# Kernel optimization log

Measured on AMD Instinct MI355X. Metric: run time of the kernel, lower is better.

## Reference

```python
import jax, jax.numpy as jnp
import numpy as np

TEMPERATURE = 0.1
EPS = 1e-8  # torch F.cosine_similarity norm clamp


def setup_inputs() -> dict:
    key = jax.random.key(0)
    k1, k2 = jax.random.split(key)
    N, D, N_CLASSES = 4096, 512, 16
    features = jax.random.normal(k1, (N, D), dtype=jnp.float32)
    labels = jax.random.randint(k2, (N,), 0, N_CLASSES, dtype=jnp.int64)
    return {"features": features, "labels": labels}


def reference(features, labels):
    N = features.shape[0]
    # cosine similarity via normalize + matmul (same math as the broadcasted
    # F.cosine_similarity, expressed as a BLAS path)
    norms = jnp.clip(jnp.linalg.norm(features, axis=1, keepdims=True), EPS)
    f = features / norms
    sim = f @ f.T  # (N, N)

    # drop the diagonal: row i keeps columns j != i, giving (N, N-1)
    j = jnp.arange(N - 1)
    cols = j[None, :] + (j[None, :] >= jnp.arange(N)[:, None])  # (N, N-1)
    sim_nd = jnp.take_along_axis(sim, cols, axis=1)

    # positive mask: same label, diagonal excluded, same column layout
    eq = labels[:, None] == labels[None, :]
    pos_nd = jnp.take_along_axis(eq, cols, axis=1)  # (N, N-1) bool

    logits = sim_nd / TEMPERATURE
    # torch.max(mask.float(), dim=1) -> first positive index per row
    targets = jnp.argmax(pos_nd.astype(jnp.float32), axis=1)  # (N,)

    logp = jax.nn.log_softmax(logits, axis=1)
    loss = -jnp.mean(jnp.take_along_axis(logp, targets[:, None], axis=1))
    return loss
```

## Files before the change

### kernel.cpp

```cpp
#include <hip/hip_runtime.h>
#include <hip/hip_bf16.h>
#include <math.h>

#define NROW 4096
#define DIM  512
#define TINV8 0.0390625f
#define EPSN 1e-8f
#define BM 128
#define BK 64
#define NB  (NROW / BM)
#define NBLK (NB * (NB + 1) / 2)

typedef float f32x4 __attribute__((ext_vector_type(4)));

__device__ __forceinline__ void gload_lds16(const void* g, void* l) {
    __builtin_amdgcn_global_load_lds(
        (const __attribute__((address_space(1))) unsigned int*)g,
        (__attribute__((address_space(3))) unsigned int*)l,
        16, 0, 0);
}

__global__ __launch_bounds__(256) void kprep(const float* __restrict__ feat,
                                             const int* __restrict__ labels,
                                             unsigned char* __restrict__ fb8,
                                             int* __restrict__ target,
                                             float* __restrict__ rowsum) {
    if (blockIdx.x < NROW / 4) {
        const int row  = blockIdx.x * 4 + (threadIdx.x >> 6);
        const int lane = threadIdx.x & 63;
        const float* rp = feat + (size_t)row * DIM + lane * 8;
        float4 v0 = *(const float4*)rp;
        float4 v1 = *(const float4*)(rp + 4);
        float ss = v0.x*v0.x + v0.y*v0.y + v0.z*v0.z + v0.w*v0.w
                 + v1.x*v1.x + v1.y*v1.y + v1.z*v1.z + v1.w*v1.w;
        #pragma unroll
        for (int m = 1; m < 64; m <<= 1) ss += __shfl_xor(ss, m);
        const float inv = 16.0f / fmaxf(sqrtf(ss), EPSN);
        int w0 = __builtin_amdgcn_cvt_pk_fp8_f32(v0.x * inv, v0.y * inv, 0, false);
        w0     = __builtin_amdgcn_cvt_pk_fp8_f32(v0.z * inv, v0.w * inv, w0, true);
        int w1 = __builtin_amdgcn_cvt_pk_fp8_f32(v1.x * inv, v1.y * inv, 0, false);
        w1     = __builtin_amdgcn_cvt_pk_fp8_f32(v1.z * inv, v1.w * inv, w1, true);
        *(int2*)(fb8 + (size_t)row * DIM + lane * 8) = make_int2(w0, w1);
    } else {
        __shared__ int firstS[16], secondS[16];
        const int t = threadIdx.x;
        if (t < 16) { firstS[t] = NROW; secondS[t] = NROW; }
        for (int i = t; i < NROW; i += 256) rowsum[i] = 0.0f;
        __syncthreads();
        for (int i = t; i < NROW; i += 256) atomicMin(&firstS[labels[i]], i);
        __syncthreads();
        for (int i = t; i < NROW; i += 256) {
            const int c = labels[i];
            if (i != firstS[c]) atomicMin(&secondS[c], i);
        }
        __syncthreads();
        for (int i = t; i < NROW; i += 256) {
            const int c = labels[i];
            int tg = (firstS[c] == i) ? secondS[c] : firstS[c];
            if (tg >= NROW) tg = (i == 0) ? 1 : 0;
            target[i] = tg;
        }
    }
}

__global__ __launch_bounds__(256) void ksim(const unsigned char* __restrict__ fb8,
                                            const int* __restrict__ target,
                                            float* __restrict__ rowsum,
                                            float* __restrict__ tlog) {
    __shared__ __align__(16) unsigned char As[2][BM * BK];
    __shared__ __align__(16) unsigned char Bs[2][BM * BK];

    int bi = 0, rem = blockIdx.x;
    while (rem >= NB - bi) { rem -= NB - bi; bi++; }
    const int bj = bi + rem;
    const bool offdiag = (bi != bj);

    const int brow = bi * BM;
    const int bcol = bj * BM;
    const int tid  = threadIdx.x;
    const int wid  = tid >> 6;
    const int lane = tid & 63;
    const int wm = wid >> 1, wn = wid & 1;

    f32x4 acc[4][4];
    #pragma unroll
    for (int m = 0; m < 4; m++)
        #pragma unroll
        for (int n = 0; n < 4; n++)
            #pragma unroll
            for (int q = 0; q < 4; q++) acc[m][n][q] = 0.0f;

    const int skey = ((lane >> 2) & 3) ^ ((lane >> 4) & 3);
    const int sc   = (lane & 3) ^ skey;

    auto STAGE = [&](int buf, int kb) {
        #pragma unroll
        for (int q = 0; q < 2; q++) {
            const int r0 = wid * 32 + q * 16;
            const unsigned char* gA = fb8 + (size_t)(brow + r0 + (lane >> 2)) * DIM + kb + sc * 16;
            const unsigned char* gB = fb8 + (size_t)(bcol + r0 + (lane >> 2)) * DIM + kb + sc * 16;
            gload_lds16(gA, &As[buf][r0 * BK]);
            gload_lds16(gB, &Bs[buf][r0 * BK]);
        }
    };

    const int ro   = lane & 15;
    const int rkey = (ro & 3) ^ ((ro >> 2) & 3);
    const int hp   = (lane >> 4) & 1;
    const int g2   = lane >> 5;

    int cur = 0;
    STAGE(cur, 0);
    __syncthreads();

    for (int t = 0; t < DIM / BK; ++t) {
        if (t + 1 < DIM / BK) STAGE(cur ^ 1, (t + 1) * BK);
        const unsigned char* Ab = As[cur];
        const unsigned char* Bb = Bs[cur];
        #pragma unroll
        for (int kk = 0; kk < 2; kk++) {
            const int p   = (kk * 2 + g2) ^ rkey;
            const int cof = (p * 2 + hp) * 8;
            long a[4], b[4];
            #pragma unroll
            for (int m = 0; m < 4; m++)
                a[m] = *(const long*)(Ab + (wm * 64 + m * 16 + ro) * BK + cof);
            #pragma unroll
            for (int n = 0; n < 4; n++)
                b[n] = *(const long*)(Bb + (wn * 64 + n * 16 + ro) * BK + cof);
            #pragma unroll
            for (int m = 0; m < 4; m++)
                #pragma unroll
                for (int n = 0; n < 4; n++)
                    acc[m][n] = __builtin_amdgcn_mfma_f32_16x16x32_fp8_fp8(a[m], b[n], acc[m][n], 0, 0, 0);
        }
        __syncthreads();
        cur ^= 1;
    }

    const int lhi = lane >> 4, llo = lane & 15;
    float colacc[4] = {0.f, 0.f, 0.f, 0.f};
    int tgj[4];
    #pragma unroll
    for (int n = 0; n < 4; n++) tgj[n] = target[bcol + wn * 64 + n * 16 + llo];

    #pragma unroll
    for (int m = 0; m < 4; m++) {
        #pragma unroll
        for (int q = 0; q < 4; q++) {
            const int i  = brow + wm * 64 + m * 16 + lhi * 4 + q;
            const int tgi = target[i];
            float psum = 0.0f;
            #pragma unroll
            for (int n = 0; n < 4; n++) {
                const int j = bcol + wn * 64 + n * 16 + llo;
                const float logit = acc[m][n][q] * TINV8;
                const float expv  = __expf(logit);
                if (j != i) psum += expv;
                if (j == tgi) tlog[i] = logit;
                if (offdiag) {
                    colacc[n] += expv;
                    if (i == tgj[n]) tlog[j] = logit;
                }
            }
            psum += __shfl_xor(psum, 1);
            psum += __shfl_xor(psum, 2);
            psum += __shfl_xor(psum, 4);
            psum += __shfl_xor(psum, 8);
            if (llo == 0) atomicAdd(&rowsum[i], psum);
        }
    }
    if (offdiag) {
        #pragma unroll
        for (int n = 0; n < 4; n++) {
            colacc[n] += __shfl_xor(colacc[n], 16);
            colacc[n] += __shfl_xor(colacc[n], 32);
            if (lhi == 0) atomicAdd(&rowsum[bcol + wn * 64 + n * 16 + llo], colacc[n]);
        }
    }
}

__global__ __launch_bounds__(256) void kloss(const float* __restrict__ rowsum,
                                             const float* __restrict__ tlog,
                                             float* __restrict__ out) {
    __shared__ float red[256];
    float s = 0.0f;
    for (int i = threadIdx.x; i < NROW; i += 256)
        s += logf(rowsum[i]) - tlog[i];
    red[threadIdx.x] = s;
    __syncthreads();
    for (int k = 128; k > 0; k >>= 1) {
        if (threadIdx.x < k) red[threadIdx.x] += red[threadIdx.x + k];
        __syncthreads();
    }
    if (threadIdx.x == 0) out[0] = red[0] / (float)NROW;
}

extern "C" void kernel_launch(void* const* d_in, const int* in_sizes, int n_in,
                              void* d_out, int out_size, void* d_ws, size_t ws_size,
                              hipStream_t stream) {
    const float* feat  = (const float*)d_in[0];
    const int* labels  = (const int*)d_in[1];
    float* out = (float*)d_out;

    char* ws = (char*)d_ws;
    unsigned char* fb8 = (unsigned char*)ws;
    float* rowsum = (float*)(ws + (size_t)NROW * DIM);
    float* tlog   = rowsum + NROW;
    int*   target = (int*)(tlog + NROW);

    kprep<<<NROW / 4 + 1, 256, 0, stream>>>(feat, labels, fb8, target, rowsum);
    ksim <<<NBLK, 256, 0, stream>>>(fb8, target, rowsum, tlog);
    kloss<<<1, 256, 0, stream>>>(rowsum, tlog, out);
}
```

Measured before the change: 43.37 us.

## Fuse final loss reduction into similarity kernel and use 8 waves per block

```diff
diff --git a/kernel.cpp b/kernel.cpp
--- a/kernel.cpp
+++ b/kernel.cpp
@@ -24,7 +24,8 @@
                                              const int* __restrict__ labels,
                                              unsigned char* __restrict__ fb8,
                                              int* __restrict__ target,
-                                             float* __restrict__ rowsum) {
+                                             float* __restrict__ rowsum,
+                                             int* __restrict__ donecnt) {
     if (blockIdx.x < NROW / 4) {
         const int row  = blockIdx.x * 4 + (threadIdx.x >> 6);
         const int lane = threadIdx.x & 63;
@@ -45,6 +46,7 @@
         __shared__ int firstS[16], secondS[16];
         const int t = threadIdx.x;
         if (t < 16) { firstS[t] = NROW; secondS[t] = NROW; }
+        if (t == 0) *donecnt = 0;
         for (int i = t; i < NROW; i += 256) rowsum[i] = 0.0f;
         __syncthreads();
         for (int i = t; i < NROW; i += 256) atomicMin(&firstS[labels[i]], i);
@@ -63,10 +65,12 @@
     }
 }
 
-__global__ __launch_bounds__(256) void ksim(const unsigned char* __restrict__ fb8,
+__global__ __launch_bounds__(512) void ksim(const unsigned char* __restrict__ fb8,
                                             const int* __restrict__ target,
                                             float* __restrict__ rowsum,
-                                            float* __restrict__ tlog) {
+                                            float* __restrict__ tlog,
+                                            int* __restrict__ donecnt,
+                                            float* __restrict__ out) {
     __shared__ __align__(16) unsigned char As[2][BM * BK];
     __shared__ __align__(16) unsigned char Bs[2][BM * BK];
 
@@ -80,28 +84,26 @@
     const int tid  = threadIdx.x;
     const int wid  = tid >> 6;
     const int lane = tid & 63;
-    const int wm = wid >> 1, wn = wid & 1;
-
-    f32x4 acc[4][4];
+    const int wm = wid >> 2;
+    const int wn = wid & 3;
+
+    f32x4 acc[4][2];
     #pragma unroll
     for (int m = 0; m < 4; m++)
         #pragma unroll
-        for (int n = 0; n < 4; n++)
+        for (int n = 0; n < 2; n++)
             #pragma unroll
             for (int q = 0; q < 4; q++) acc[m][n][q] = 0.0f;
 
     const int skey = ((lane >> 2) & 3) ^ ((lane >> 4) & 3);
     const int sc   = (lane & 3) ^ skey;
+    const int srow = wid * 16 + (lane >> 2);
 
     auto STAGE = [&](int buf, int kb) {
-        #pragma unroll
-        for (int q = 0; q < 2; q++) {
-            const int r0 = wid * 32 + q * 16;
-            const unsigned char* gA = fb8 + (size_t)(brow + r0 + (lane >> 2)) * DIM + kb + sc * 16;
-            const unsigned char* gB = fb8 + (size_t)(bcol + r0 + (lane >> 2)) * DIM + kb + sc * 16;
-            gload_lds16(gA, &As[buf][r0 * BK]);
-            gload_lds16(gB, &Bs[buf][r0 * BK]);
-        }
+        const unsigned char* gA = fb8 + (size_t)(brow + srow) * DIM + kb + sc * 16;
+        const unsigned char* gB = fb8 + (size_t)(bcol + srow) * DIM + kb + sc * 16;
+        gload_lds16(gA, &As[buf][(wid * 16) * BK]);
+        gload_lds16(gB, &Bs[buf][(wid * 16) * BK]);
     };
 
     const int ro   = lane & 15;
@@ -121,17 +123,17 @@
         for (int kk = 0; kk < 2; kk++) {
             const int p   = (kk * 2 + g2) ^ rkey;
             const int cof = (p * 2 + hp) * 8;
-            long a[4], b[4];
+            long a[4], b[2];
             #pragma unroll
             for (int m = 0; m < 4; m++)
                 a[m] = *(const long*)(Ab + (wm * 64 + m * 16 + ro) * BK + cof);
             #pragma unroll
-            for (int n = 0; n < 4; n++)
-                b[n] = *(const long*)(Bb + (wn * 64 + n * 16 + ro) * BK + cof);
+            for (int n = 0; n < 2; n++)
+                b[n] = *(const long*)(Bb + (wn * 32 + n * 16 + ro) * BK + cof);
             #pragma unroll
             for (int m = 0; m < 4; m++)
                 #pragma unroll
-                for (int n = 0; n < 4; n++)
+                for (int n = 0; n < 2; n++)
                     acc[m][n] = __builtin_amdgcn_mfma_f32_16x16x32_fp8_fp8(a[m], b[n], acc[m][n], 0, 0, 0);
         }
         __syncthreads();
@@ -139,10 +141,10 @@
     }
 
     const int lhi = lane >> 4, llo = lane & 15;
-    float colacc[4] = {0.f, 0.f, 0.f, 0.f};
-    int tgj[4];
+    float colacc[2] = {0.f, 0.f};
+    int tgj[2];
     #pragma unroll
-    for (int n = 0; n < 4; n++) tgj[n] = target[bcol + wn * 64 + n * 16 + llo];
+    for (int n = 0; n < 2; n++) tgj[n] = target[bcol + wn * 32 + n * 16 + llo];
 
     #pragma unroll
     for (int m = 0; m < 4; m++) {
@@ -152,8 +154,8 @@
             const int tgi = target[i];
             float psum = 0.0f;
             #pragma unroll
-            for (int n = 0; n < 4; n++) {
-                const int j = bcol + wn * 64 + n * 16 + llo;
+            for (int n = 0; n < 2; n++) {
+                const int j = bcol + wn * 32 + n * 16 + llo;
                 const float logit = acc[m][n][q] * TINV8;
                 const float expv  = __expf(logit);
                 if (j != i) psum += expv;
@@ -172,28 +174,31 @@
     }
     if (offdiag) {
         #pragma unroll
-        for (int n = 0; n < 4; n++) {
+        for (int n = 0; n < 2; n++) {
             colacc[n] += __shfl_xor(colacc[n], 16);
             colacc[n] += __shfl_xor(colacc[n], 32);
-            if (lhi == 0) atomicAdd(&rowsum[bcol + wn * 64 + n * 16 + llo], colacc[n]);
-        }
-    }
-}
-
-__global__ __launch_bounds__(256) void kloss(const float* __restrict__ rowsum,
-                                             const float* __restrict__ tlog,
-                                             float* __restrict__ out) {
-    __shared__ float red[256];
+            if (lhi == 0) atomicAdd(&rowsum[bcol + wn * 32 + n * 16 + llo], colacc[n]);
+        }
+    }
+
+    __threadfence();
+    __shared__ int lastS;
+    if (tid == 0) lastS = (atomicAdd(donecnt, 1) == NBLK - 1);
+    __syncthreads();
+    if (!lastS) return;
+    __threadfence();
+
     float s = 0.0f;
-    for (int i = threadIdx.x; i < NROW; i += 256)
-        s += logf(rowsum[i]) - tlog[i];
-    red[threadIdx.x] = s;
+    for (int i = tid; i < NROW; i += 512)
+        s += __logf(rowsum[i]) - tlog[i];
+    float* red = (float*)As;
+    red[tid] = s;
     __syncthreads();
-    for (int k = 128; k > 0; k >>= 1) {
-        if (threadIdx.x < k) red[threadIdx.x] += red[threadIdx.x + k];
-        __syncthreads();
-    }
-    if (threadIdx.x == 0) out[0] = red[0] / (float)NROW;
+    for (int k = 256; k > 0; k >>= 1) {
+        if (tid < k) red[tid] += red[tid + k];
+        __syncthreads();
+    }
+    if (tid == 0) out[0] = red[0] / (float)NROW;
 }
 
 extern "C" void kernel_launch(void* const* d_in, const int* in_sizes, int n_in,
@@ -208,8 +213,8 @@
     float* rowsum = (float*)(ws + (size_t)NROW * DIM);
     float* tlog   = rowsum + NROW;
     int*   target = (int*)(tlog + NROW);
-
-    kprep<<<NROW / 4 + 1, 256, 0, stream>>>(feat, labels, fb8, target, rowsum);
-    ksim <<<NBLK, 256, 0, stream>>>(fb8, target, rowsum, tlog);
-    kloss<<<1, 256, 0, stream>>>(rowsum, tlog, out);
-}
+    int*   donecnt = target + NROW;
+
+    kprep<<<NROW / 4 + 1, 256, 0, stream>>>(feat, labels, fb8, target, rowsum, donecnt);
+    ksim <<<NBLK, 512, 0, stream>>>(fb8, target, rowsum, tlog, donecnt, out);
+}
```

Result: slower. 103.8 us (+139.4%).
